# Kernel optimization log

Measured on AMD Instinct MI355X. Metric: run time of the kernel, lower is better.

The kernel has to match this reference:

```python
import jax, jax.numpy as jnp
import numpy as np

B, L, H, E, D = 2, 2048, 8, 64, 64

def setup_inputs() -> dict:
    key = jax.random.key(0)
    kq, kk, kv, ks = jax.random.split(key, 4)
    return {
        "queries": jax.random.normal(kq, (B, L, H, E), dtype=jnp.float32),
        "keys": jax.random.normal(kk, (B, L, H, E), dtype=jnp.float32),
        "values": jax.random.normal(kv, (B, L, H, D), dtype=jnp.float32),
        "sigma": jax.random.normal(ks, (B, L, H), dtype=jnp.float32),
    }

def reference(queries, keys, values, sigma):
    b, l, h, e = queries.shape
    scale = 1.0 / np.sqrt(e).astype(np.float32)
    # raw attention scores [B,H,L,S]
    scores = jnp.einsum('blhe,bshe->bhls', queries, keys)
    # strict causal mask (mask j > i)
    causal = jnp.triu(jnp.ones((l, l), dtype=bool), k=1)
    scores = jnp.where(causal[None, None], -jnp.inf, scores)
    attn = scale * scores
    # learned Gaussian prior per query-key distance
    sig = jnp.transpose(sigma, (0, 2, 1))            # [B,H,L]
    sig = jax.nn.sigmoid(sig * 5.0) + 1e-5
    sig = jnp.power(3.0, sig) - 1.0                  # in (0, 2)
    sig = sig[..., None]                             # [B,H,L,1] broadcast over window
    idx = jnp.arange(l, dtype=jnp.float32)
    dist = jnp.abs(idx[:, None] - idx[None, :])      # [L,L]
    inv_sqrt_2pi = 1.0 / np.sqrt(2.0 * np.pi).astype(np.float32)
    prior = (inv_sqrt_2pi / sig) * jnp.exp(-(dist[None, None] ** 2) / (2.0 * sig ** 2))  # [B,H,L,L]
    series = jax.nn.softmax(attn, axis=-1)           # [B,H,L,S]
    V = jnp.einsum('bhls,bshd->blhd', series, values)  # [B,L,H,D]
    sigma_out = jnp.broadcast_to(sig, prior.shape)
    return V, series, prior, sigma_out
```

## Files before the change

### kernel.cpp

```cpp
#include <hip/hip_runtime.h>

#define L_ 2048
#define H_ 8

typedef __attribute__((ext_vector_type(8))) short short8;
typedef __attribute__((ext_vector_type(4))) float f32x4;

static constexpr size_t OFF_S = 2097152;
static constexpr size_t OFF_P = OFF_S + 67108864;
static constexpr size_t OFF_G = OFF_P + 67108864;

static constexpr size_t WS_K = 1u << 20;
static constexpr size_t WS_V = WS_K + (4u << 20);

__device__ __forceinline__ unsigned short f2bf(float x) {
    union { float f; unsigned int u; } c; c.f = x;
    unsigned int u = c.u;
    u += 0x7fffu + ((u >> 16) & 1u);
    return (unsigned short)(u >> 16);
}
__device__ __forceinline__ float bf2f(unsigned short u) {
    union { float f; unsigned int v; } c; c.v = ((unsigned int)u) << 16; return c.f;
}

__device__ __forceinline__ void gld_lds16(const unsigned short* g, unsigned short* l) {
    __builtin_amdgcn_global_load_lds(
        (const __attribute__((address_space(1))) void*)g,
        (__attribute__((address_space(3))) void*)l, 16, 0, 0);
}

__global__ __launch_bounds__(256) void prep(
    const float* __restrict__ k, const float* __restrict__ v,
    unsigned short* __restrict__ wsK, unsigned short* __restrict__ wsV)
{
    const int tid = threadIdx.x;
    const int blk = blockIdx.x;
    __shared__ __attribute__((aligned(16))) unsigned short tr[64][72];
    if (blk < 512) {
        const int bh = blk >> 5, t = blk & 31;
        const int b = bh >> 3, h = bh & 7;
        unsigned short* dst = wsK + (size_t)(bh * 32 + t) * 4096;
        #pragma unroll
        for (int p = 0; p < 2; ++p) {
            const int cid = tid + (p << 8);
            const int r = cid >> 3, c = cid & 7;
            const int j = (t << 6) + r;
            const float4* src = reinterpret_cast<const float4*>(
                k + (((size_t)((b * L_ + j) * H_ + h)) << 6) + (c << 3));
            float4 x0 = src[0], x1 = src[1];
            union { short8 s; unsigned short u[8]; } w;
            w.u[0]=f2bf(x0.x); w.u[1]=f2bf(x0.y); w.u[2]=f2bf(x0.z); w.u[3]=f2bf(x0.w);
            w.u[4]=f2bf(x1.x); w.u[5]=f2bf(x1.y); w.u[6]=f2bf(x1.z); w.u[7]=f2bf(x1.w);
            *reinterpret_cast<short8*>(dst + r * 64 + ((c ^ (r & 7)) << 3)) = w.s;
        }
    } else {
        const int vb = blk - 512;
        const int bh = vb >> 5, t = vb & 31;
        const int b = bh >> 3, h = bh & 7;
        const int col4 = (tid & 15) << 2;
        #pragma unroll
        for (int p = 0; p < 4; ++p) {
            const int r = (tid >> 4) + (p << 4);
            const int j = (t << 6) + r;
            float4 x = *reinterpret_cast<const float4*>(
                v + (((size_t)((b * L_ + j) * H_ + h)) << 6) + col4);
            tr[col4 + 0][r] = f2bf(x.x); tr[col4 + 1][r] = f2bf(x.y);
            tr[col4 + 2][r] = f2bf(x.z); tr[col4 + 3][r] = f2bf(x.w);
        }
        __syncthreads();
        unsigned short* dst = wsV + (size_t)(bh * 32 + t) * 4096;
        #pragma unroll
        for (int p = 0; p < 2; ++p) {
            const int cid = tid + (p << 8);
            const int d = cid >> 3, cj = cid & 7;
            short8 s = *reinterpret_cast<const short8*>(&tr[d][cj << 3]);
            *reinterpret_cast<short8*>(dst + d * 64 + ((cj ^ (d & 7)) << 3)) = s;
        }
    }
}

__global__ __launch_bounds__(256) void attn(
    const float* __restrict__ q,
    const unsigned short* __restrict__ wsK, const unsigned short* __restrict__ wsV,
    float* __restrict__ out, float* __restrict__ ws_inv)
{
    __shared__ __attribute__((aligned(16))) unsigned short Kb[2][4096];
    __shared__ __attribute__((aligned(16))) unsigned short Vb[2][4096];
    __shared__ __attribute__((aligned(16))) unsigned short Pt[16][72];
    __shared__ float l_sums[16];

    const int tid  = threadIdx.x;
    const int wv   = tid >> 6;
    const int lane = tid & 63;
    const int quad = lane >> 4;
    const int l16  = lane & 15;

    const int blk = blockIdx.x;
    const int s   = 127 - (blk >> 4);
    const int bh  = blk & 15;
    const int b   = bh >> 3, h = bh & 7;
    const int i0  = s << 4;

    if (tid < 16) l_sums[tid] = 0.0f;

    short8 a0, a1;
    {
        const float* qr = q + (((size_t)((b * L_ + (i0 + l16)) * H_ + h)) << 6);
        const float4* q4 = reinterpret_cast<const float4*>(qr) + quad * 2;
        float4 x0 = q4[0], x1 = q4[1];
        float4 y0 = q4[8], y1 = q4[9];
        union { short8 v8; unsigned short u[8]; } fa, fb;
        fa.u[0]=f2bf(x0.x); fa.u[1]=f2bf(x0.y); fa.u[2]=f2bf(x0.z); fa.u[3]=f2bf(x0.w);
        fa.u[4]=f2bf(x1.x); fa.u[5]=f2bf(x1.y); fa.u[6]=f2bf(x1.z); fa.u[7]=f2bf(x1.w);
        fb.u[0]=f2bf(y0.x); fb.u[1]=f2bf(y0.y); fb.u[2]=f2bf(y0.z); fb.u[3]=f2bf(y0.w);
        fb.u[4]=f2bf(y1.x); fb.u[5]=f2bf(y1.y); fb.u[6]=f2bf(y1.z); fb.u[7]=f2bf(y1.w);
        a0 = fa.v8; a1 = fb.v8;
    }

    const int ntiles = (s >> 2) + 1;
    const unsigned short* gK = wsK + ((size_t)bh * 32) * 4096;
    const unsigned short* gV = wsV + ((size_t)bh * 32) * 4096;

    #define STAGE(buf, t) do {                                              \
        const unsigned short* _sk = gK + (size_t)(t) * 4096;                \
        const unsigned short* _sv = gV + (size_t)(t) * 4096;                \
        _Pragma("unroll")                                                   \
        for (int _qq = 0; _qq < 2; ++_qq) {                                 \
            const int _off = (wv << 10) + (_qq << 9);                       \
            gld_lds16(_sk + _off + (lane << 3), &Kb[buf][_off]);            \
            gld_lds16(_sv + _off + (lane << 3), &Vb[buf][_off]);            \
        }                                                                   \
    } while (0)

    f32x4 oacc = {0.f, 0.f, 0.f, 0.f};
    float lpart[4] = {0.f, 0.f, 0.f, 0.f};
    float* outS = out + OFF_S;
    const int r = (wv << 4) + l16;

    STAGE(0, 0);
    for (int t = 0; t < ntiles; ++t) {
        const int p = t & 1;
        __syncthreads();
        if (t + 1 < ntiles) STAGE(1 - p, t + 1);
        const int j0 = t << 6;
        short8 b0 = *reinterpret_cast<const short8*>(&Kb[p][r * 64 + ((quad ^ (r & 7)) << 3)]);
        short8 b1 = *reinterpret_cast<const short8*>(&Kb[p][r * 64 + (((quad + 4) ^ (r & 7)) << 3)]);
        f32x4 c4 = {0.f, 0.f, 0.f, 0.f};
        c4 = __builtin_amdgcn_mfma_f32_16x16x32_bf16(a0, b0, c4, 0, 0, 0);
        c4 = __builtin_amdgcn_mfma_f32_16x16x32_bf16(a1, b1, c4, 0, 0, 0);
        const int j = j0 + r;
        #pragma unroll
        for (int rr = 0; rr < 4; ++rr) {
            const int i = i0 + (quad << 2) + rr;
            float pv = (j <= i) ? __expf(c4[rr] * 0.125f - 8.0f) : 0.0f;
            lpart[rr] += pv;
            Pt[(quad << 2) + rr][r] = f2bf(pv);
        }
        __syncthreads();
        short8 pa0 = *reinterpret_cast<const short8*>(&Pt[l16][quad << 3]);
        short8 pa1 = *reinterpret_cast<const short8*>(&Pt[l16][32 + (quad << 3)]);
        short8 vb0 = *reinterpret_cast<const short8*>(&Vb[p][r * 64 + ((quad ^ (r & 7)) << 3)]);
        short8 vb1 = *reinterpret_cast<const short8*>(&Vb[p][r * 64 + (((quad + 4) ^ (r & 7)) << 3)]);
        oacc = __builtin_amdgcn_mfma_f32_16x16x32_bf16(pa0, vb0, oacc, 0, 0, 0);
        oacc = __builtin_amdgcn_mfma_f32_16x16x32_bf16(pa1, vb1, oacc, 0, 0, 0);
        const int srow = tid >> 4, scol = (tid & 15) << 2;
        const unsigned short* pp = &Pt[srow][scol];
        float4 pf = { bf2f(pp[0]), bf2f(pp[1]), bf2f(pp[2]), bf2f(pp[3]) };
        *reinterpret_cast<float4*>(outS + (((size_t)(bh * L_ + i0 + srow)) << 11) + j0 + scol) = pf;
    }
    #undef STAGE

    #pragma unroll
    for (int rr = 0; rr < 4; ++rr) {
        float x = lpart[rr];
        x += __shfl_xor(x, 1); x += __shfl_xor(x, 2);
        x += __shfl_xor(x, 4); x += __shfl_xor(x, 8);
        if (l16 == 0) atomicAdd(&l_sums[(quad << 2) + rr], x);
    }
    __syncthreads();
    #pragma unroll
    for (int rr = 0; rr < 4; ++rr) {
        const int i = i0 + (quad << 2) + rr;
        const float inv = 1.0f / l_sums[(quad << 2) + rr];
        out[(((size_t)((b * L_ + i) * H_ + h)) << 6) + (wv << 4) + l16] = oacc[rr] * inv;
    }
    if (tid < 16) ws_inv[(bh << 11) + i0 + tid] = 1.0f / l_sums[tid];
}

__global__ __launch_bounds__(256) void finish(
    const float* __restrict__ sg, const float* __restrict__ ws_inv,
    float* __restrict__ out)
{
    __shared__ float sA[4], sC2[4], sS[4], sI[4];
    const int tid = threadIdx.x;
    const int g0 = blockIdx.x << 2;
    if (tid < 4) {
        const int g = g0 + tid;
        const int bh = g >> 11, i = g & 2047, b = bh >> 3, h = bh & 7;
        const float x = sg[(size_t)((b * L_ + i) * H_ + h)];
        const float sgm = 1.0f / (1.0f + __expf(-5.0f * x)) + 1e-5f;
        const float sp = expm1f(sgm * 1.0986122886681098f);
        sS[tid] = sp;
        sA[tid] = 0.3989422804014327f / sp;
        sC2[tid] = 0.5f / (sp * sp);
        sI[tid] = ws_inv[g];
    }
    __syncthreads();
    float* outS = out + OFF_S;
    float* outP = out + OFF_P;
    float* outG = out + OFF_G;
    #pragma unroll
    for (int rr = 0; rr < 4; ++rr) {
        const int g = g0 + rr;
        const int i = g & 2047;
        const size_t base = (size_t)g << 11;
        const float A = sA[rr], C2 = sC2[rr], S = sS[rr], I = sI[rr];
        #pragma unroll
        for (int p = 0; p < 2; ++p) {
            const int c = (tid + (p << 8)) << 2;
            const float d0 = (float)(i - c);
            const float d1 = d0 - 1.f, d2 = d0 - 2.f, d3 = d0 - 3.f;
            float4 pr;
            pr.x = A * __expf(-d0 * d0 * C2);
            pr.y = A * __expf(-d1 * d1 * C2);
            pr.z = A * __expf(-d2 * d2 * C2);
            pr.w = A * __expf(-d3 * d3 * C2);
            *reinterpret_cast<float4*>(outP + base + c) = pr;
            float4 sv = {S, S, S, S};
            *reinterpret_cast<float4*>(outG + base + c) = sv;
            float4 se;
            if (c + 3 <= i) {
                se = *reinterpret_cast<const float4*>(outS + base + c);
                se.x *= I; se.y *= I; se.z *= I; se.w *= I;
            } else if (c > i) {
                se.x = 0.f; se.y = 0.f; se.z = 0.f; se.w = 0.f;
            } else {
                const float4 t4 = *reinterpret_cast<const float4*>(outS + base + c);
                se.x = (c     <= i) ? t4.x * I : 0.f;
                se.y = (c + 1 <= i) ? t4.y * I : 0.f;
                se.z = (c + 2 <= i) ? t4.z * I : 0.f;
                se.w = (c + 3 <= i) ? t4.w * I : 0.f;
            }
            *reinterpret_cast<float4*>(outS + base + c) = se;
        }
    }
}

extern "C" void kernel_launch(void* const* d_in, const int* in_sizes, int n_in,
                              void* d_out, int out_size, void* d_ws, size_t ws_size,
                              hipStream_t stream) {
    const float* q  = (const float*)d_in[0];
    const float* k  = (const float*)d_in[1];
    const float* v  = (const float*)d_in[2];
    const float* sg = (const float*)d_in[3];
    float* outp = (float*)d_out;
    float* ws_inv = (float*)d_ws;
    unsigned short* wsK = (unsigned short*)((char*)d_ws + WS_K);
    unsigned short* wsV = (unsigned short*)((char*)d_ws + WS_V);
    prep<<<dim3(1024), dim3(256), 0, stream>>>(k, v, wsK, wsV);
    attn<<<dim3(2048), dim3(256), 0, stream>>>(q, wsK, wsV, outp, ws_inv);
    finish<<<dim3(8192), dim3(256), 0, stream>>>(sg, ws_inv, outp);
}
```

Baseline: 892.2 us.

## Stage unnormalized probabilities as bf16 in workspace, double query rows per block

The attention kernel now processes 32 query rows per block instead of 16, so each staged K/V tile is reused twice. The block order also changes to pair heavy and light causal rows. Unnormalized probabilities are written as bf16 to a workspace buffer rather than as fp32 into the series output, which halves that intermediate traffic and removes the read-modify-write of the output in the finish kernel. Barriers become explicit waitcnt/s_barrier sequences so the next tile's prefetch can stay in flight, and the finish kernel handles 8 rows per block with 8 columns per thread. The risks are larger per-block register use, a workspace buffer at a fixed 16 MB offset, and hand-written synchronisation that must stay correct.

New measurement: 935.0 us. +4.8%, slower.

```diff
diff --git a/kernel.cpp b/kernel.cpp
--- a/kernel.cpp
+++ b/kernel.cpp
@@ -12,6 +12,7 @@
 
 static constexpr size_t WS_K = 1u << 20;
 static constexpr size_t WS_V = WS_K + (4u << 20);
+static constexpr size_t WS_P = 16u << 20;
 
 __device__ __forceinline__ unsigned short f2bf(float x) {
     union { float f; unsigned int u; } c; c.f = x;
@@ -82,12 +83,12 @@
 __global__ __launch_bounds__(256) void attn(
     const float* __restrict__ q,
     const unsigned short* __restrict__ wsK, const unsigned short* __restrict__ wsV,
-    float* __restrict__ out, float* __restrict__ ws_inv)
+    float* __restrict__ out, float* __restrict__ ws_inv, unsigned short* __restrict__ wsP)
 {
     __shared__ __attribute__((aligned(16))) unsigned short Kb[2][4096];
     __shared__ __attribute__((aligned(16))) unsigned short Vb[2][4096];
-    __shared__ __attribute__((aligned(16))) unsigned short Pt[16][72];
-    __shared__ float l_sums[16];
+    __shared__ __attribute__((aligned(16))) unsigned short Pt[32][72];
+    __shared__ float l_sums[32];
 
     const int tid  = threadIdx.x;
     const int wv   = tid >> 6;
@@ -96,34 +97,42 @@
     const int l16  = lane & 15;
 
     const int blk = blockIdx.x;
-    const int s   = 127 - (blk >> 4);
+    const int s   = (blk < 512) ? (63 - (blk >> 4)) : ((blk - 512) >> 4);
     const int bh  = blk & 15;
     const int b   = bh >> 3, h = bh & 7;
-    const int i0  = s << 4;
-
-    if (tid < 16) l_sums[tid] = 0.0f;
-
-    short8 a0, a1;
+    const int i0  = s << 5;
+
+    if (tid < 32) l_sums[tid] = 0.0f;
+    __syncthreads();
+
+    short8 a0l, a1l, a0h, a1h;
     {
         const float* qr = q + (((size_t)((b * L_ + (i0 + l16)) * H_ + h)) << 6);
         const float4* q4 = reinterpret_cast<const float4*>(qr) + quad * 2;
-        float4 x0 = q4[0], x1 = q4[1];
-        float4 y0 = q4[8], y1 = q4[9];
+        float4 x0 = q4[0], x1 = q4[1], y0 = q4[8], y1 = q4[9];
         union { short8 v8; unsigned short u[8]; } fa, fb;
         fa.u[0]=f2bf(x0.x); fa.u[1]=f2bf(x0.y); fa.u[2]=f2bf(x0.z); fa.u[3]=f2bf(x0.w);
         fa.u[4]=f2bf(x1.x); fa.u[5]=f2bf(x1.y); fa.u[6]=f2bf(x1.z); fa.u[7]=f2bf(x1.w);
         fb.u[0]=f2bf(y0.x); fb.u[1]=f2bf(y0.y); fb.u[2]=f2bf(y0.z); fb.u[3]=f2bf(y0.w);
         fb.u[4]=f2bf(y1.x); fb.u[5]=f2bf(y1.y); fb.u[6]=f2bf(y1.z); fb.u[7]=f2bf(y1.w);
-        a0 = fa.v8; a1 = fb.v8;
-    }
-
-    const int ntiles = (s >> 2) + 1;
-    const unsigned short* gK = wsK + ((size_t)bh * 32) * 4096;
-    const unsigned short* gV = wsV + ((size_t)bh * 32) * 4096;
+        a0l = fa.v8; a1l = fb.v8;
+        const float* qr2 = qr + (16ll * H_ << 6);
+        const float4* q42 = reinterpret_cast<const float4*>(qr2) + quad * 2;
+        x0 = q42[0]; x1 = q42[1]; y0 = q42[8]; y1 = q42[9];
+        fa.u[0]=f2bf(x0.x); fa.u[1]=f2bf(x0.y); fa.u[2]=f2bf(x0.z); fa.u[3]=f2bf(x0.w);
+        fa.u[4]=f2bf(x1.x); fa.u[5]=f2bf(x1.y); fa.u[6]=f2bf(x1.z); fa.u[7]=f2bf(x1.w);
+        fb.u[0]=f2bf(y0.x); fb.u[1]=f2bf(y0.y); fb.u[2]=f2bf(y0.z); fb.u[3]=f2bf(y0.w);
+        fb.u[4]=f2bf(y1.x); fb.u[5]=f2bf(y1.y); fb.u[6]=f2bf(y1.z); fb.u[7]=f2bf(y1.w);
+        a0h = fa.v8; a1h = fb.v8;
+    }
+
+    const int ntiles = (s >> 1) + 1;
+    const unsigned short* gK = wsK + ((size_t)bh << 17);
+    const unsigned short* gV = wsV + ((size_t)bh << 17);
 
     #define STAGE(buf, t) do {                                              \
-        const unsigned short* _sk = gK + (size_t)(t) * 4096;                \
-        const unsigned short* _sv = gV + (size_t)(t) * 4096;                \
+        const unsigned short* _sk = gK + ((size_t)(t) << 12);               \
+        const unsigned short* _sv = gV + ((size_t)(t) << 12);               \
         _Pragma("unroll")                                                   \
         for (int _qq = 0; _qq < 2; ++_qq) {                                 \
             const int _off = (wv << 10) + (_qq << 9);                       \
@@ -132,69 +141,83 @@
         }                                                                   \
     } while (0)
 
-    f32x4 oacc = {0.f, 0.f, 0.f, 0.f};
-    float lpart[4] = {0.f, 0.f, 0.f, 0.f};
-    float* outS = out + OFF_S;
-    const int r = (wv << 4) + l16;
+    f32x4 oacc0 = {0.f,0.f,0.f,0.f}, oacc1 = {0.f,0.f,0.f,0.f};
+    float lp[8];
+    #pragma unroll
+    for (int z = 0; z < 8; ++z) lp[z] = 0.f;
+    const int r  = (wv << 4) + l16;
+    const int xr = r & 7;
 
     STAGE(0, 0);
     for (int t = 0; t < ntiles; ++t) {
         const int p = t & 1;
-        __syncthreads();
+        if (t == 0) asm volatile("s_waitcnt vmcnt(0)\n\ts_barrier" ::: "memory");
+        else        asm volatile("s_waitcnt vmcnt(1)\n\ts_barrier" ::: "memory");
         if (t + 1 < ntiles) STAGE(1 - p, t + 1);
         const int j0 = t << 6;
-        short8 b0 = *reinterpret_cast<const short8*>(&Kb[p][r * 64 + ((quad ^ (r & 7)) << 3)]);
-        short8 b1 = *reinterpret_cast<const short8*>(&Kb[p][r * 64 + (((quad + 4) ^ (r & 7)) << 3)]);
-        f32x4 c4 = {0.f, 0.f, 0.f, 0.f};
-        c4 = __builtin_amdgcn_mfma_f32_16x16x32_bf16(a0, b0, c4, 0, 0, 0);
-        c4 = __builtin_amdgcn_mfma_f32_16x16x32_bf16(a1, b1, c4, 0, 0, 0);
+        const unsigned short* kb = &Kb[p][r << 6];
+        short8 b0 = *reinterpret_cast<const short8*>(kb + ((quad ^ xr) << 3));
+        short8 b1 = *reinterpret_cast<const short8*>(kb + (((quad + 4) ^ xr) << 3));
         const int j = j0 + r;
         #pragma unroll
-        for (int rr = 0; rr < 4; ++rr) {
-            const int i = i0 + (quad << 2) + rr;
-            float pv = (j <= i) ? __expf(c4[rr] * 0.125f - 8.0f) : 0.0f;
-            lpart[rr] += pv;
-            Pt[(quad << 2) + rr][r] = f2bf(pv);
-        }
-        __syncthreads();
-        short8 pa0 = *reinterpret_cast<const short8*>(&Pt[l16][quad << 3]);
-        short8 pa1 = *reinterpret_cast<const short8*>(&Pt[l16][32 + (quad << 3)]);
-        short8 vb0 = *reinterpret_cast<const short8*>(&Vb[p][r * 64 + ((quad ^ (r & 7)) << 3)]);
-        short8 vb1 = *reinterpret_cast<const short8*>(&Vb[p][r * 64 + (((quad + 4) ^ (r & 7)) << 3)]);
-        oacc = __builtin_amdgcn_mfma_f32_16x16x32_bf16(pa0, vb0, oacc, 0, 0, 0);
-        oacc = __builtin_amdgcn_mfma_f32_16x16x32_bf16(pa1, vb1, oacc, 0, 0, 0);
-        const int srow = tid >> 4, scol = (tid & 15) << 2;
-        const unsigned short* pp = &Pt[srow][scol];
-        float4 pf = { bf2f(pp[0]), bf2f(pp[1]), bf2f(pp[2]), bf2f(pp[3]) };
-        *reinterpret_cast<float4*>(outS + (((size_t)(bh * L_ + i0 + srow)) << 11) + j0 + scol) = pf;
+        for (int g = 0; g < 2; ++g) {
+            f32x4 c4 = {0.f,0.f,0.f,0.f};
+            c4 = __builtin_amdgcn_mfma_f32_16x16x32_bf16(g ? a0h : a0l, b0, c4, 0, 0, 0);
+            c4 = __builtin_amdgcn_mfma_f32_16x16x32_bf16(g ? a1h : a1l, b1, c4, 0, 0, 0);
+            #pragma unroll
+            for (int rr = 0; rr < 4; ++rr) {
+                const int i = i0 + (g << 4) + (quad << 2) + rr;
+                float pv = (j <= i) ? __expf(c4[rr] * 0.125f - 8.0f) : 0.0f;
+                lp[(g << 2) + rr] += pv;
+                Pt[(g << 4) + (quad << 2) + rr][r] = f2bf(pv);
+            }
+        }
+        asm volatile("s_waitcnt lgkmcnt(0)\n\ts_barrier" ::: "memory");
+        const unsigned short* vb = &Vb[p][r << 6];
+        short8 vb0 = *reinterpret_cast<const short8*>(vb + ((quad ^ xr) << 3));
+        short8 vb1 = *reinterpret_cast<const short8*>(vb + (((quad + 4) ^ xr) << 3));
+        short8 pa0l = *reinterpret_cast<const short8*>(&Pt[l16][quad << 3]);
+        short8 pa1l = *reinterpret_cast<const short8*>(&Pt[l16][32 + (quad << 3)]);
+        short8 pa0h = *reinterpret_cast<const short8*>(&Pt[16 + l16][quad << 3]);
+        short8 pa1h = *reinterpret_cast<const short8*>(&Pt[16 + l16][32 + (quad << 3)]);
+        oacc0 = __builtin_amdgcn_mfma_f32_16x16x32_bf16(pa0l, vb0, oacc0, 0, 0, 0);
+        oacc0 = __builtin_amdgcn_mfma_f32_16x16x32_bf16(pa1l, vb1, oacc0, 0, 0, 0);
+        oacc1 = __builtin_amdgcn_mfma_f32_16x16x32_bf16(pa0h, vb0, oacc1, 0, 0, 0);
+        oacc1 = __builtin_amdgcn_mfma_f32_16x16x32_bf16(pa1h, vb1, oacc1, 0, 0, 0);
+        const int srow = tid >> 3, scol = (tid & 7) << 3;
+        short8 sv = *reinterpret_cast<const short8*>(&Pt[srow][scol]);
+        *reinterpret_cast<short8*>(wsP + (((size_t)(bh * L_ + i0 + srow)) << 11) + j0 + scol) = sv;
     }
     #undef STAGE
 
     #pragma unroll
-    for (int rr = 0; rr < 4; ++rr) {
-        float x = lpart[rr];
+    for (int z = 0; z < 8; ++z) {
+        float x = lp[z];
         x += __shfl_xor(x, 1); x += __shfl_xor(x, 2);
         x += __shfl_xor(x, 4); x += __shfl_xor(x, 8);
-        if (l16 == 0) atomicAdd(&l_sums[(quad << 2) + rr], x);
+        if (l16 == 0) atomicAdd(&l_sums[((z >> 2) << 4) + (quad << 2) + (z & 3)], x);
     }
     __syncthreads();
     #pragma unroll
-    for (int rr = 0; rr < 4; ++rr) {
-        const int i = i0 + (quad << 2) + rr;
-        const float inv = 1.0f / l_sums[(quad << 2) + rr];
-        out[(((size_t)((b * L_ + i) * H_ + h)) << 6) + (wv << 4) + l16] = oacc[rr] * inv;
-    }
-    if (tid < 16) ws_inv[(bh << 11) + i0 + tid] = 1.0f / l_sums[tid];
+    for (int z = 0; z < 8; ++z) {
+        const int g = z >> 2, rr = z & 3;
+        const int row = (g << 4) + (quad << 2) + rr;
+        const int i = i0 + row;
+        const float inv = 1.0f / l_sums[row];
+        const float ov = (g ? oacc1[rr] : oacc0[rr]) * inv;
+        out[(((size_t)((b * L_ + i) * H_ + h)) << 6) + (wv << 4) + l16] = ov;
+    }
+    if (tid < 32) ws_inv[(bh << 11) + i0 + tid] = 1.0f / l_sums[tid];
 }
 
 __global__ __launch_bounds__(256) void finish(
     const float* __restrict__ sg, const float* __restrict__ ws_inv,
-    float* __restrict__ out)
+    const unsigned short* __restrict__ wsP, float* __restrict__ out)
 {
-    __shared__ float sA[4], sC2[4], sS[4], sI[4];
+    __shared__ float sA[8], sC2[8], sS[8], sI[8];
     const int tid = threadIdx.x;
-    const int g0 = blockIdx.x << 2;
-    if (tid < 4) {
+    const int g0 = blockIdx.x << 3;
+    if (tid < 8) {
         const int g = g0 + tid;
         const int bh = g >> 11, i = g & 2047, b = bh >> 3, h = bh & 7;
         const float x = sg[(size_t)((b * L_ + i) * H_ + h)];
@@ -209,40 +232,41 @@
     float* outS = out + OFF_S;
     float* outP = out + OFF_P;
     float* outG = out + OFF_G;
-    #pragma unroll
-    for (int rr = 0; rr < 4; ++rr) {
+    const int c0 = tid << 3;
+    #pragma unroll
+    for (int rr = 0; rr < 8; ++rr) {
         const int g = g0 + rr;
         const int i = g & 2047;
         const size_t base = (size_t)g << 11;
         const float A = sA[rr], C2 = sC2[rr], S = sS[rr], I = sI[rr];
-        #pragma unroll
-        for (int p = 0; p < 2; ++p) {
-            const int c = (tid + (p << 8)) << 2;
-            const float d0 = (float)(i - c);
-            const float d1 = d0 - 1.f, d2 = d0 - 2.f, d3 = d0 - 3.f;
-            float4 pr;
-            pr.x = A * __expf(-d0 * d0 * C2);
-            pr.y = A * __expf(-d1 * d1 * C2);
-            pr.z = A * __expf(-d2 * d2 * C2);
-            pr.w = A * __expf(-d3 * d3 * C2);
-            *reinterpret_cast<float4*>(outP + base + c) = pr;
-            float4 sv = {S, S, S, S};
-            *reinterpret_cast<float4*>(outG + base + c) = sv;
-            float4 se;
-            if (c + 3 <= i) {
-                se = *reinterpret_cast<const float4*>(outS + base + c);
-                se.x *= I; se.y *= I; se.z *= I; se.w *= I;
-            } else if (c > i) {
-                se.x = 0.f; se.y = 0.f; se.z = 0.f; se.w = 0.f;
-            } else {
-                const float4 t4 = *reinterpret_cast<const float4*>(outS + base + c);
-                se.x = (c     <= i) ? t4.x * I : 0.f;
-                se.y = (c + 1 <= i) ? t4.y * I : 0.f;
-                se.z = (c + 2 <= i) ? t4.z * I : 0.f;
-                se.w = (c + 3 <= i) ? t4.w * I : 0.f;
-            }
-            *reinterpret_cast<float4*>(outS + base + c) = se;
-        }
+        union { short8 s; unsigned short u[8]; } pw;
+        pw.s = *reinterpret_cast<const short8*>(wsP + base + c0);
+        float4 s0, s1;
+        s0.x = (c0 + 0 <= i) ? bf2f(pw.u[0]) * I : 0.f;
+        s0.y = (c0 + 1 <= i) ? bf2f(pw.u[1]) * I : 0.f;
+        s0.z = (c0 + 2 <= i) ? bf2f(pw.u[2]) * I : 0.f;
+        s0.w = (c0 + 3 <= i) ? bf2f(pw.u[3]) * I : 0.f;
+        s1.x = (c0 + 4 <= i) ? bf2f(pw.u[4]) * I : 0.f;
+        s1.y = (c0 + 5 <= i) ? bf2f(pw.u[5]) * I : 0.f;
+        s1.z = (c0 + 6 <= i) ? bf2f(pw.u[6]) * I : 0.f;
+        s1.w = (c0 + 7 <= i) ? bf2f(pw.u[7]) * I : 0.f;
+        *reinterpret_cast<float4*>(outS + base + c0)     = s0;
+        *reinterpret_cast<float4*>(outS + base + c0 + 4) = s1;
+        const float d0 = (float)(i - c0);
+        float4 p0, p1;
+        p0.x = A * __expf(-d0 * d0 * C2);
+        { float d = d0 - 1.f; p0.y = A * __expf(-d * d * C2); }
+        { float d = d0 - 2.f; p0.z = A * __expf(-d * d * C2); }
+        { float d = d0 - 3.f; p0.w = A * __expf(-d * d * C2); }
+        { float d = d0 - 4.f; p1.x = A * __expf(-d * d * C2); }
+        { float d = d0 - 5.f; p1.y = A * __expf(-d * d * C2); }
+        { float d = d0 - 6.f; p1.z = A * __expf(-d * d * C2); }
+        { float d = d0 - 7.f; p1.w = A * __expf(-d * d * C2); }
+        *reinterpret_cast<float4*>(outP + base + c0)     = p0;
+        *reinterpret_cast<float4*>(outP + base + c0 + 4) = p1;
+        float4 sv = {S, S, S, S};
+        *reinterpret_cast<float4*>(outG + base + c0)     = sv;
+        *reinterpret_cast<float4*>(outG + base + c0 + 4) = sv;
     }
 }
 
@@ -257,7 +281,8 @@
     float* ws_inv = (float*)d_ws;
     unsigned short* wsK = (unsigned short*)((char*)d_ws + WS_K);
     unsigned short* wsV = (unsigned short*)((char*)d_ws + WS_V);
+    unsigned short* wsP = (unsigned short*)((char*)d_ws + WS_P);
     prep<<<dim3(1024), dim3(256), 0, stream>>>(k, v, wsK, wsV);
-    attn<<<dim3(2048), dim3(256), 0, stream>>>(q, wsK, wsV, outp, ws_inv);
-    finish<<<dim3(8192), dim3(256), 0, stream>>>(sg, ws_inv, outp);
-}
+    attn<<<dim3(1024), dim3(256), 0, stream>>>(q, wsK, wsV, outp, ws_inv, wsP);
+    finish<<<dim3(4096), dim3(256), 0, stream>>>(sg, ws_inv, wsP, outp);
+}
```
